# Kernel optimization log

Hardware: AMD Instinct MI355X
Metric: run time of the kernel (lower is better)

## Reference

```python
import math
import jax, jax.numpy as jnp
import numpy as np

H, KV, D = 16, 4, 128          # num_heads, num_kv_heads, head_dim
HID = 2048                      # hidden_size
ROPE_BASE = 1e6
EPS = 1e-6


def setup_inputs() -> dict:
    key = jax.random.key(0)
    ks = jax.random.split(key, 3)
    B, S = 2, 2048
    s = 0.02
    return {
        "x": jax.random.normal(ks[0], (B, S, HID), jnp.float32),
        "w_qkv": jax.random.normal(ks[1], (2 * H * D + 2 * KV * D, HID), jnp.float32) * s,
        "w_o": jax.random.normal(ks[2], (HID, H * D), jnp.float32) * s,
        "q_norm_w": jnp.ones((D,), jnp.float32),
        "q_norm_b": jnp.zeros((D,), jnp.float32),
        "k_norm_w": jnp.ones((D,), jnp.float32),
        "k_norm_b": jnp.zeros((D,), jnp.float32),
    }


def _layernorm(x, w, b):
    mu = jnp.mean(x, axis=-1, keepdims=True)
    xc = x - mu
    var = jnp.mean(xc * xc, axis=-1, keepdims=True)
    return xc * jax.lax.rsqrt(var + EPS) * w + b


def _rope(x, cos, sin):
    # x: [B, h, S, D]; cos/sin: [S, D/2]; interleaved real/imag pairs
    xr, xi = x[..., 0::2], x[..., 1::2]
    c, s = cos[None, None], sin[None, None]
    out = jnp.stack([xr * c - xi * s, xr * s + xi * c], axis=-1)
    return out.reshape(x.shape)


def reference(x, w_qkv, w_o, q_norm_w, q_norm_b, k_norm_w, k_norm_b):
    B, S, _ = x.shape
    qkv = x @ w_qkv.T                                  # [B,S,2*H*D+2*KV*D]
    qg, k, v = jnp.split(qkv, [2 * H * D, 2 * H * D + KV * D], axis=-1)
    q, gate = jnp.split(qg, 2, axis=-1)                # [B,S,H*D] each

    q = q.reshape(B, S, H, D).transpose(0, 2, 1, 3)    # [B,H,S,D]
    k = k.reshape(B, S, KV, D).transpose(0, 2, 1, 3)   # [B,KV,S,D]
    v = v.reshape(B, S, KV, D).transpose(0, 2, 1, 3)

    q = _layernorm(q, q_norm_w, q_norm_b)
    k = _layernorm(k, k_norm_w, k_norm_b)

    inv = 1.0 / (ROPE_BASE ** (jnp.arange(0, D, 2, dtype=jnp.float32) / D))
    freqs = jnp.outer(jnp.arange(S, dtype=jnp.float32), inv)  # [S, D/2]
    cos, sin = jnp.cos(freqs), jnp.sin(freqs)
    q = _rope(q, cos, sin)
    k = _rope(k, cos, sin)

    rep = H // KV
    k = jnp.repeat(k, rep, axis=1)                     # [B,H,S,D]
    v = jnp.repeat(v, rep, axis=1)

    scores = jnp.einsum('bhqd,bhkd->bhqk', q, k) / math.sqrt(D)
    causal = jnp.tril(jnp.ones((S, S), bool))
    scores = jnp.where(causal[None, None], scores, -jnp.inf)
    attn = jax.nn.softmax(scores, axis=-1)
    out = jnp.einsum('bhqk,bhkd->bhqd', attn, v)
    out = out.transpose(0, 2, 1, 3).reshape(B, S, H * D)
    out = out * jax.nn.sigmoid(gate)
    return out @ w_o.T
```

## Files before the change

### kernel.cpp

```cpp
#include <hip/hip_runtime.h>
#include <hip/hip_bf16.h>

typedef __bf16 bf16_t;
typedef __bf16 bf16x2 __attribute__((ext_vector_type(2)));
typedef __bf16 bf16x4v __attribute__((ext_vector_type(4)));
typedef __bf16 bf16x8 __attribute__((ext_vector_type(8)));
typedef float f32x4 __attribute__((ext_vector_type(4)));

#define LOG2E 1.4426950408889634f
#define QSCALE (0.08838834764831843f * 1.4426950408889634f)

__global__ __launch_bounds__(256) void cvt_f32_bf16(const float* __restrict__ in,
                                                    bf16_t* __restrict__ out, int n4) {
  int i = blockIdx.x * 256 + threadIdx.x;
  if (i < n4) {
    float4 v = ((const float4*)in)[i];
    bf16x4v o;
    o[0] = (__bf16)v.x; o[1] = (__bf16)v.y; o[2] = (__bf16)v.z; o[3] = (__bf16)v.w;
    *(bf16x4v*)(out + (size_t)i * 4) = o;
  }
}

__global__ __launch_bounds__(256) void rope_tables(float* __restrict__ cosT,
                                                   float* __restrict__ sinT) {
  int idx = blockIdx.x * 256 + threadIdx.x;
  int s = idx >> 6, i = idx & 63;
  float inv = __builtin_amdgcn_exp2f(-(float)i * (19.931568569324174f / 64.0f));
  float f = (float)s * inv;
  cosT[idx] = cosf(f);
  sinT[idx] = sinf(f);
}

template<int MI, int NI>
__global__ __launch_bounds__(512) void gemm8p(const bf16_t* __restrict__ A,
                                              const bf16_t* __restrict__ B,
                                              float* __restrict__ C,
                                              int M, int N, int K) {
  constexpr int BM = MI * 32;
  constexpr int BN = NI * 64;
  constexpr int NA = BM / 64;
  constexpr int NB = BN / 64;
  constexpr int ST = NA + NB;
  constexpr int PH = MI / 2;

  __shared__ bf16_t LA[2][BM * 64];
  __shared__ bf16_t LB[2][BN * 64];

  int nb = N / BN;
  int cpx = gridDim.x >> 3;
  int bid = blockIdx.x;
  int swz = (bid & 7) * cpx + (bid >> 3);
  int bm = swz / nb, bn = swz % nb;
  int m0 = bm * BM, n0 = bn * BN;
  int tid = threadIdx.x, lane = tid & 63, wv = tid >> 6;
  int wr = wv >> 2, wc = wv & 3, lr = lane & 15, g = lane >> 4;
  int T = K >> 6;

  auto stageI = [&](int kt, int bi, int s) {
    int k0 = kt << 6;
    if (s < NA) {
      int c = s * 512 + tid;
      int row = c >> 3, lc = (c & 7) ^ (row & 7);
      __builtin_amdgcn_global_load_lds(
          (const __attribute__((address_space(1))) void*)(A + (size_t)(m0 + row) * K + k0 + lc * 8),
          (__attribute__((address_space(3))) void*)&LA[bi][(s * 512 + wv * 64) * 8], 16, 0, 0);
    } else {
      int c = (s - NA) * 512 + tid;
      int row = c >> 3, lc = (c & 7) ^ (row & 7);
      __builtin_amdgcn_global_load_lds(
          (const __attribute__((address_space(1))) void*)(B + (size_t)(n0 + row) * K + k0 + lc * 8),
          (__attribute__((address_space(3))) void*)&LB[bi][((s - NA) * 512 + wv * 64) * 8], 16, 0, 0);
    }
  };

  f32x4 acc[MI][NI];
#pragma unroll
  for (int i = 0; i < MI; i++)
#pragma unroll
    for (int j = 0; j < NI; j++)
#pragma unroll
      for (int r = 0; r < 4; r++) acc[i][j][r] = 0.f;

#pragma unroll
  for (int s = 0; s < ST; s++) stageI(0, 0, s);

  int ofk0 = ((0 + g) ^ (lr & 7)) << 3;
  int ofk1 = ((4 + g) ^ (lr & 7)) << 3;
  int offA = (wr * (MI * 16) + lr) * 64;
  int offB = (wc * (NI * 16) + lr) * 64;

  for (int t = 0; t < T; t++) {
    int bi = t & 1, bo = bi ^ 1;
    const bf16_t* la = LA[bi];
    const bf16_t* lb = LB[bi];
    bool pre = (t + 1 < T);
    if (pre) {
#pragma unroll
      for (int s = 0; s < ST; s++) stageI(t + 1, bo, s);
      if constexpr (ST == 9) asm volatile("s_waitcnt vmcnt(9)" ::: "memory");
      else                   asm volatile("s_waitcnt vmcnt(6)" ::: "memory");
    } else {
      asm volatile("s_waitcnt vmcnt(0)" ::: "memory");
    }
    __builtin_amdgcn_s_barrier();
    asm volatile("" ::: "memory");
    bf16x8 bq[NI];
#pragma unroll
    for (int ph = 0; ph < PH; ph++) {
      const int ks = (PH == 4) ? (ph >> 1) : ph;
      const int q  = (PH == 4) ? (ph & 1) : 0;
      const bool rb = (PH == 2) || ((ph & 1) == 0);
      const int ofk = ks ? ofk1 : ofk0;
      bf16x8 af[4];
#pragma unroll
      for (int i = 0; i < 4; i++)
        af[i] = *(const bf16x8*)&la[offA + (q * 4 + i) * 1024 + ofk];
      if (rb) {
#pragma unroll
        for (int ni = 0; ni < NI; ni++)
          bq[ni] = *(const bf16x8*)&lb[offB + ni * 1024 + ofk];
      }
      if (ph != 0) {
        asm volatile("" ::: "memory");
        __builtin_amdgcn_s_barrier();
        asm volatile("" ::: "memory");
      }
      __builtin_amdgcn_s_setprio(1);
#pragma unroll
      for (int i = 0; i < 4; i++)
#pragma unroll
        for (int ni = 0; ni < NI; ni++)
          acc[q * 4 + i][ni] =
              __builtin_amdgcn_mfma_f32_16x16x32_bf16(af[i], bq[ni], acc[q * 4 + i][ni], 0, 0, 0);
      __builtin_amdgcn_s_setprio(0);
      asm volatile("s_waitcnt lgkmcnt(0)" ::: "memory");
      __builtin_amdgcn_s_barrier();
      asm volatile("" ::: "memory");
    }
  }

#pragma unroll
  for (int mi = 0; mi < MI; mi++)
#pragma unroll
    for (int ni = 0; ni < NI; ni++) {
      int m = m0 + wr * (MI * 16) + mi * 16 + g * 4;
      int n = n0 + wc * (NI * 16) + ni * 16 + lr;
#pragma unroll
      for (int r = 0; r < 4; r++) C[(size_t)(m + r) * N + n] = acc[mi][ni][r];
    }
}

__global__ __launch_bounds__(256) void ln_rope(const float* __restrict__ qkv,
                                               const float* __restrict__ qw, const float* __restrict__ qb,
                                               const float* __restrict__ kw, const float* __restrict__ kb,
                                               const float* __restrict__ cosT, const float* __restrict__ sinT,
                                               bf16_t* __restrict__ Qr, bf16_t* __restrict__ Kr) {
  int row = blockIdx.x;
  int b = row >> 11, s = row & 2047;
  int lane = threadIdx.x & 63, wv = threadIdx.x >> 6;
  float c = cosT[(s << 6) + lane], sn = sinT[(s << 6) + lane];
  const float* base = qkv + (size_t)row * 5120;
#pragma unroll
  for (int i = 0; i < 5; i++) {
    int head = wv * 5 + i;
    bool isq = head < 16;
    int off = isq ? (head << 7) : (4096 + ((head - 16) << 7));
    float2 x = *(const float2*)(base + off + (lane << 1));
    float sum = x.x + x.y;
#pragma unroll
    for (int m = 1; m < 64; m <<= 1) sum += __shfl_xor(sum, m);
    float mu = sum * 0.0078125f;
    float x0 = x.x - mu, x1 = x.y - mu;
    float vs = x0 * x0 + x1 * x1;
#pragma unroll
    for (int m = 1; m < 64; m <<= 1) vs += __shfl_xor(vs, m);
    float rs = rsqrtf(vs * 0.0078125f + 1e-6f);
    const float* w = isq ? qw : kw;
    const float* bb = isq ? qb : kb;
    float y0 = x0 * rs * w[lane << 1] + bb[lane << 1];
    float y1 = x1 * rs * w[(lane << 1) + 1] + bb[(lane << 1) + 1];
    float o0 = y0 * c - y1 * sn;
    float o1 = y0 * sn + y1 * c;
    if (isq) { o0 *= QSCALE; o1 *= QSCALE; }
    bf16x2 ov; ov[0] = (__bf16)o0; ov[1] = (__bf16)o1;
    size_t dst = isq ? ((((size_t)(b * 16 + head)) * 2048 + s) * 128 + (lane << 1))
                     : ((((size_t)(b * 4 + (head - 16))) * 2048 + s) * 128 + (lane << 1));
    *(bf16x2*)((isq ? Qr : Kr) + dst) = ov;
  }
}

__global__ __launch_bounds__(256) void vtrans(const float* __restrict__ qkv,
                                              bf16_t* __restrict__ Vt) {
  int bid = blockIdx.x;
  int sb = bid & 63, kv = (bid >> 6) & 3, b = bid >> 8;
  int s0 = sb << 5;
  __shared__ bf16_t T[128 * 33];
  int tid = threadIdx.x;
#pragma unroll
  for (int i = 0; i < 16; i++) {
    int idx = i * 256 + tid;
    int r = idx >> 7, d = idx & 127;
    float v = qkv[((size_t)(b * 2048 + s0 + r)) * 5120 + 4608 + (kv << 7) + d];
    T[d * 33 + r] = (__bf16)v;
  }
  __syncthreads();
#pragma unroll
  for (int j = 0; j < 16; j++) {
    int idx = j * 256 + tid;
    int d = idx >> 5, sc = idx & 31;
    Vt[(((size_t)(b * 4 + kv)) * 128 + d) * 2048 + s0 + sc] = T[d * 33 + sc];
  }
}

__global__ __launch_bounds__(256, 3) void attn(const bf16_t* __restrict__ Qr,
                                               const bf16_t* __restrict__ Kr,
                                               const bf16_t* __restrict__ Vt,
                                               const float* __restrict__ qkv,
                                               bf16_t* __restrict__ ag) {
  __shared__ bf16_t Ks[2][32 * 128];
  __shared__ bf16_t Vs[2][128 * 32];
  int bid = blockIdx.x;
  int hb = bid & 31;
  int h = hb & 15, b = hb >> 4;
  int pr = bid >> 5;
  int kvh = h >> 2;
  int tid = threadIdx.x, lane = tid & 63, wv = tid >> 6;
  int lr = lane & 15, g = lane >> 4;
  int r0base = ((lr >> 2) << 3) + (lr & 3);

  const bf16_t* Kg = Kr + ((size_t)(b * 4 + kvh)) * 2048 * 128;
  const bf16_t* Vg = Vt + ((size_t)(b * 4 + kvh)) * 128 * 2048;

  auto stage = [&](int buf, int kv0) {
#pragma unroll
    for (int i = 0; i < 2; i++) {
      int c = i * 256 + tid;
      int row = c >> 4, lc = (c & 15) ^ (row & 15);
      __builtin_amdgcn_global_load_lds(
          (const __attribute__((address_space(1))) void*)(Kg + (size_t)(kv0 + row) * 128 + lc * 8),
          (__attribute__((address_space(3))) void*)&Ks[buf][c * 8], 16, 0, 0);
    }
#pragma unroll
    for (int i = 0; i < 2; i++) {
      int c = i * 256 + tid;
      int d = c >> 2, cv = (c & 3) ^ ((d >> 1) & 3);
      __builtin_amdgcn_global_load_lds(
          (const __attribute__((address_space(1))) void*)(Vg + (size_t)d * 2048 + kv0 + cv * 8),
          (__attribute__((address_space(3))) void*)&Vs[buf][c * 8], 16, 0, 0);
    }
  };

  auto sm = [&](const f32x4& s0, const f32x4& s1, int qrow, int kvabs, bool dia,
                float& mrun, float& lsp, bf16x8& pb, f32x4 (&oac)[8]) {
    float tt[8];
#pragma unroll
    for (int r = 0; r < 4; r++) { tt[r] = s0[r]; tt[4 + r] = s1[r]; }
    if (dia) {
#pragma unroll
      for (int r = 0; r < 4; r++) {
        if (kvabs + r > qrow)     tt[r]     = -1e30f;
        if (kvabs + 4 + r > qrow) tt[4 + r] = -1e30f;
      }
    }
    float lm = fmaxf(fmaxf(fmaxf(tt[0], tt[1]), tt[2]),
                     fmaxf(fmaxf(tt[3], tt[4]), fmaxf(fmaxf(tt[5], tt[6]), tt[7])));
    if (__all(lm <= mrun + 8.f)) {
      float ps = 0.f;
#pragma unroll
      for (int i = 0; i < 8; i++) {
        float pv = __builtin_amdgcn_exp2f(tt[i] - mrun);
        pb[i] = (__bf16)pv; ps += pv;
      }
      lsp += ps;
    } else {
      float pm = lm;
      pm = fmaxf(pm, __shfl_xor(pm, 16));
      pm = fmaxf(pm, __shfl_xor(pm, 32));
      float mnew = fmaxf(mrun, pm);
      float corr = __builtin_amdgcn_exp2f(mrun - mnew);
      float ps = 0.f;
#pragma unroll
      for (int i = 0; i < 8; i++) {
        float pv = __builtin_amdgcn_exp2f(tt[i] - mnew);
        pb[i] = (__bf16)pv; ps += pv;
      }
      lsp = lsp * corr + ps;
      mrun = mnew;
#pragma unroll
      for (int dt = 0; dt < 8; dt++)
#pragma unroll
        for (int r = 0; r < 4; r++) oac[dt][r] *= corr;
    }
  };

  for (int phase = 0; phase < 2; phase++) {
    int qb = phase ? (31 - pr) : pr;
    int qw0 = qb << 6;
    int qw = qw0 + (wv << 4);
    int qrow = qw + lr;
    int qmax = qw + 15;
    int nt = (qb + 1) << 1;

    const bf16_t* Qg = Qr + (((size_t)(b * 16 + h)) * 2048 + qrow) * 128;
    bf16x8 qf[4];
#pragma unroll
    for (int ds = 0; ds < 4; ds++) qf[ds] = *(const bf16x8*)(Qg + ds * 32 + g * 8);

    f32x4 oa[8];
#pragma unroll
    for (int i = 0; i < 8; i++)
#pragma unroll
      for (int r = 0; r < 4; r++) oa[i][r] = 0.f;
    float mrun = -1e30f, lsp = 0.f;

    stage(0, 0);
    for (int t = 0; t < nt; t++) {
      int cur = t & 1;
      if (t + 1 < nt) {
        stage(cur ^ 1, (t + 1) << 5);
        asm volatile("s_waitcnt vmcnt(4)" ::: "memory");
      } else {
        asm volatile("s_waitcnt vmcnt(0)" ::: "memory");
      }
      __builtin_amdgcn_s_barrier();
      asm volatile("" ::: "memory");
      int kvb = t << 5;
      if (kvb <= qmax) {
        const bf16_t* kb = Ks[cur];
        const bf16_t* vb = Vs[cur];
        int ra = r0base, rb2 = r0base + 4;
        bf16x8 a0[4], a1[4];
#pragma unroll
        for (int ds = 0; ds < 4; ds++) {
          a0[ds] = *(const bf16x8*)&kb[ra * 128 + (((ds * 4 + g) ^ (ra & 15)) << 3)];
          a1[ds] = *(const bf16x8*)&kb[rb2 * 128 + (((ds * 4 + g) ^ (rb2 & 15)) << 3)];
        }
        f32x4 s0, s1;
#pragma unroll
        for (int r = 0; r < 4; r++) { s0[r] = 0.f; s1[r] = 0.f; }
        __builtin_amdgcn_s_setprio(1);
#pragma unroll
        for (int ds = 0; ds < 4; ds++) {
          s0 = __builtin_amdgcn_mfma_f32_16x16x32_bf16(a0[ds], qf[ds], s0, 0, 0, 0);
          s1 = __builtin_amdgcn_mfma_f32_16x16x32_bf16(a1[ds], qf[ds], s1, 0, 0, 0);
        }
        __builtin_amdgcn_s_setprio(0);
        int kvabs = kvb + (g << 3);
        bool dia = (kvb + 31 > qw);
        bf16x8 pb;
        sm(s0, s1, qrow, kvabs, dia, mrun, lsp, pb, oa);
        __builtin_amdgcn_s_setprio(1);
#pragma unroll
        for (int dt = 0; dt < 8; dt++) {
          int d = dt * 16 + lr;
          bf16x8 va = *(const bf16x8*)&vb[d * 32 + ((g ^ ((d >> 1) & 3)) << 3)];
          oa[dt] = __builtin_amdgcn_mfma_f32_16x16x32_bf16(va, pb, oa[dt], 0, 0, 0);
        }
        __builtin_amdgcn_s_setprio(0);
      }
      asm volatile("s_waitcnt lgkmcnt(0)" ::: "memory");
      __builtin_amdgcn_s_barrier();
      asm volatile("" ::: "memory");
    }

    float ls = lsp + __shfl_xor(lsp, 16);
    ls += __shfl_xor(ls, 32);
    float invl = __builtin_amdgcn_rcpf(ls);

    size_t ob = ((size_t)b * 2048 + qrow) * 2048 + (h << 7);
    size_t gb = ((size_t)b * 2048 + qrow) * 5120 + 2048 + (h << 7);
#pragma unroll
    for (int dt = 0; dt < 8; dt++) {
      int d = dt * 16 + (g << 2);
      float4 gt = *(const float4*)(qkv + gb + d);
      bf16x4v o;
      o[0] = (__bf16)(oa[dt][0] * invl * __builtin_amdgcn_rcpf(1.f + __builtin_amdgcn_exp2f(-gt.x * LOG2E)));
      o[1] = (__bf16)(oa[dt][1] * invl * __builtin_amdgcn_rcpf(1.f + __builtin_amdgcn_exp2f(-gt.y * LOG2E)));
      o[2] = (__bf16)(oa[dt][2] * invl * __builtin_amdgcn_rcpf(1.f + __builtin_amdgcn_exp2f(-gt.z * LOG2E)));
      o[3] = (__bf16)(oa[dt][3] * invl * __builtin_amdgcn_rcpf(1.f + __builtin_amdgcn_exp2f(-gt.w * LOG2E)));
      *(bf16x4v*)(ag + ob + d) = o;
    }
  }
}

extern "C" void kernel_launch(void* const* d_in, const int* in_sizes, int n_in,
                              void* d_out, int out_size, void* d_ws, size_t ws_size,
                              hipStream_t stream) {
  const float* x    = (const float*)d_in[0];
  const float* wqkv = (const float*)d_in[1];
  const float* wo   = (const float*)d_in[2];
  const float* qnw  = (const float*)d_in[3];
  const float* qnb  = (const float*)d_in[4];
  const float* knw  = (const float*)d_in[5];
  const float* knb  = (const float*)d_in[6];
  float* out = (float*)d_out;

  char* p = (char*)d_ws;
  bf16_t* xb  = (bf16_t*)p;
  bf16_t* ag  = xb;
  p += (size_t)16777216;
  bf16_t* wqb = (bf16_t*)p;
  bf16_t* Qr  = wqb;
  p += (size_t)20971520;
  bf16_t* wob = (bf16_t*)p; p += (size_t)8388608;
  float*  qkv = (float*)p;  p += (size_t)83886080;
  bf16_t* Kr  = (bf16_t*)p; p += (size_t)4194304;
  bf16_t* Vt  = (bf16_t*)p; p += (size_t)4194304;
  float* cosT = (float*)p;  p += (size_t)524288;
  float* sinT = (float*)p;  p += (size_t)524288;

  cvt_f32_bf16<<<8192, 256, 0, stream>>>(x, xb, 2097152);
  cvt_f32_bf16<<<10240, 256, 0, stream>>>(wqkv, wqb, 2621440);
  cvt_f32_bf16<<<4096, 256, 0, stream>>>(wo, wob, 1048576);
  rope_tables<<<512, 256, 0, stream>>>(cosT, sinT);

  gemm8p<8, 5><<<256, 512, 0, stream>>>(xb, wqb, qkv, 4096, 5120, 2048);

  ln_rope<<<4096, 256, 0, stream>>>(qkv, qnw, qnb, knw, knb, cosT, sinT, Qr, Kr);
  vtrans<<<512, 256, 0, stream>>>(qkv, Vt);

  attn<<<512, 256, 0, stream>>>(Qr, Kr, Vt, qkv, ag);

  gemm8p<4, 4><<<256, 512, 0, stream>>>(ag, wob, out, 4096, 2048, 2048);
}
```

Baseline: 255.0 us.

## Restructure GEMM into four-phase ping-pong schedule with register prefetch of fragments

Replaces the templated 8-phase GEMM with a fixed BM=128 kernel whose K-step runs in four MFMA phases. LDS fragment reads for the next phase and the next tile are issued before the current MFMAs, so shared-memory latency overlaps compute. Global loads for tile t+1 are now waited on with vmcnt(0) only at the end of the iteration. The QKV projection moves from 256-row tiles on 256 blocks to 128-row tiles on 512 blocks, which adds tile count and reuses each loaded tile less.

New measurement: 287.6 us. 1.13x slower.

```diff
diff --git a/kernel.cpp b/kernel.cpp
--- a/kernel.cpp
+++ b/kernel.cpp
@@ -31,17 +31,16 @@
   sinT[idx] = sinf(f);
 }
 
-template<int MI, int NI>
-__global__ __launch_bounds__(512) void gemm8p(const bf16_t* __restrict__ A,
+template<int NI>
+__global__ __launch_bounds__(512) void gemm4p(const bf16_t* __restrict__ A,
                                               const bf16_t* __restrict__ B,
                                               float* __restrict__ C,
                                               int M, int N, int K) {
-  constexpr int BM = MI * 32;
+  constexpr int BM = 128;
   constexpr int BN = NI * 64;
-  constexpr int NA = BM / 64;
-  constexpr int NB = BN / 64;
+  constexpr int NA = 2;
+  constexpr int NB = NI;
   constexpr int ST = NA + NB;
-  constexpr int PH = MI / 2;
 
   __shared__ bf16_t LA[2][BM * 64];
   __shared__ bf16_t LB[2][BN * 64];
@@ -73,77 +72,103 @@
     }
   };
 
-  f32x4 acc[MI][NI];
-#pragma unroll
-  for (int i = 0; i < MI; i++)
+  f32x4 acc[4][NI];
+#pragma unroll
+  for (int i = 0; i < 4; i++)
 #pragma unroll
     for (int j = 0; j < NI; j++)
 #pragma unroll
       for (int r = 0; r < 4; r++) acc[i][j][r] = 0.f;
-
-#pragma unroll
-  for (int s = 0; s < ST; s++) stageI(0, 0, s);
 
   int ofk0 = ((0 + g) ^ (lr & 7)) << 3;
   int ofk1 = ((4 + g) ^ (lr & 7)) << 3;
-  int offA = (wr * (MI * 16) + lr) * 64;
+  int offA = (wr * 64 + lr) * 64;
   int offB = (wc * (NI * 16) + lr) * 64;
+
+#pragma unroll
+  for (int s = 0; s < ST; s++) stageI(0, 0, s);
+  asm volatile("s_waitcnt vmcnt(0)" ::: "memory");
+  __builtin_amdgcn_s_barrier();
+  asm volatile("" ::: "memory");
+
+  bf16x8 afA[2], afB[2], bqA[NI], bqB[NI];
+#pragma unroll
+  for (int i = 0; i < 2; i++) afA[i] = *(const bf16x8*)&LA[0][offA + i * 1024 + ofk0];
+#pragma unroll
+  for (int ni = 0; ni < NI; ni++) bqA[ni] = *(const bf16x8*)&LB[0][offB + ni * 1024 + ofk0];
 
   for (int t = 0; t < T; t++) {
     int bi = t & 1, bo = bi ^ 1;
     const bf16_t* la = LA[bi];
     const bf16_t* lb = LB[bi];
+    const bf16_t* lan = LA[bo];
+    const bf16_t* lbn = LB[bo];
     bool pre = (t + 1 < T);
+
     if (pre) {
 #pragma unroll
       for (int s = 0; s < ST; s++) stageI(t + 1, bo, s);
-      if constexpr (ST == 9) asm volatile("s_waitcnt vmcnt(9)" ::: "memory");
-      else                   asm volatile("s_waitcnt vmcnt(6)" ::: "memory");
-    } else {
-      asm volatile("s_waitcnt vmcnt(0)" ::: "memory");
-    }
+    }
+#pragma unroll
+    for (int i = 0; i < 2; i++) afB[i] = *(const bf16x8*)&la[offA + (2 + i) * 1024 + ofk0];
+    __builtin_amdgcn_s_setprio(1);
+#pragma unroll
+    for (int i = 0; i < 2; i++)
+#pragma unroll
+      for (int ni = 0; ni < NI; ni++)
+        acc[i][ni] = __builtin_amdgcn_mfma_f32_16x16x32_bf16(afA[i], bqA[ni], acc[i][ni], 0, 0, 0);
+    __builtin_amdgcn_s_setprio(0);
+    __builtin_amdgcn_s_barrier();
+
+#pragma unroll
+    for (int i = 0; i < 2; i++) afA[i] = *(const bf16x8*)&la[offA + i * 1024 + ofk1];
+#pragma unroll
+    for (int ni = 0; ni < NI; ni++) bqB[ni] = *(const bf16x8*)&lb[offB + ni * 1024 + ofk1];
+    __builtin_amdgcn_s_setprio(1);
+#pragma unroll
+    for (int i = 0; i < 2; i++)
+#pragma unroll
+      for (int ni = 0; ni < NI; ni++)
+        acc[2 + i][ni] = __builtin_amdgcn_mfma_f32_16x16x32_bf16(afB[i], bqA[ni], acc[2 + i][ni], 0, 0, 0);
+    __builtin_amdgcn_s_setprio(0);
+    __builtin_amdgcn_s_barrier();
+
+#pragma unroll
+    for (int i = 0; i < 2; i++) afB[i] = *(const bf16x8*)&la[offA + (2 + i) * 1024 + ofk1];
+    __builtin_amdgcn_s_setprio(1);
+#pragma unroll
+    for (int i = 0; i < 2; i++)
+#pragma unroll
+      for (int ni = 0; ni < NI; ni++)
+        acc[i][ni] = __builtin_amdgcn_mfma_f32_16x16x32_bf16(afA[i], bqB[ni], acc[i][ni], 0, 0, 0);
+    __builtin_amdgcn_s_setprio(0);
+    __builtin_amdgcn_s_barrier();
+
+    if (pre) asm volatile("s_waitcnt vmcnt(0)" ::: "memory");
     __builtin_amdgcn_s_barrier();
     asm volatile("" ::: "memory");
-    bf16x8 bq[NI];
-#pragma unroll
-    for (int ph = 0; ph < PH; ph++) {
-      const int ks = (PH == 4) ? (ph >> 1) : ph;
-      const int q  = (PH == 4) ? (ph & 1) : 0;
-      const bool rb = (PH == 2) || ((ph & 1) == 0);
-      const int ofk = ks ? ofk1 : ofk0;
-      bf16x8 af[4];
-#pragma unroll
-      for (int i = 0; i < 4; i++)
-        af[i] = *(const bf16x8*)&la[offA + (q * 4 + i) * 1024 + ofk];
-      if (rb) {
-#pragma unroll
-        for (int ni = 0; ni < NI; ni++)
-          bq[ni] = *(const bf16x8*)&lb[offB + ni * 1024 + ofk];
-      }
-      if (ph != 0) {
-        asm volatile("" ::: "memory");
-        __builtin_amdgcn_s_barrier();
-        asm volatile("" ::: "memory");
-      }
-      __builtin_amdgcn_s_setprio(1);
-#pragma unroll
-      for (int i = 0; i < 4; i++)
-#pragma unroll
-        for (int ni = 0; ni < NI; ni++)
-          acc[q * 4 + i][ni] =
-              __builtin_amdgcn_mfma_f32_16x16x32_bf16(af[i], bq[ni], acc[q * 4 + i][ni], 0, 0, 0);
-      __builtin_amdgcn_s_setprio(0);
-      asm volatile("s_waitcnt lgkmcnt(0)" ::: "memory");
-      __builtin_amdgcn_s_barrier();
-      asm volatile("" ::: "memory");
-    }
-  }
-
-#pragma unroll
-  for (int mi = 0; mi < MI; mi++)
+    if (pre) {
+#pragma unroll
+      for (int i = 0; i < 2; i++) afA[i] = *(const bf16x8*)&lan[offA + i * 1024 + ofk0];
+#pragma unroll
+      for (int ni = 0; ni < NI; ni++) bqA[ni] = *(const bf16x8*)&lbn[offB + ni * 1024 + ofk0];
+    }
+    __builtin_amdgcn_s_setprio(1);
+#pragma unroll
+    for (int i = 0; i < 2; i++)
+#pragma unroll
+      for (int ni = 0; ni < NI; ni++)
+        acc[2 + i][ni] = __builtin_amdgcn_mfma_f32_16x16x32_bf16(afB[i], bqB[ni], acc[2 + i][ni], 0, 0, 0);
+    __builtin_amdgcn_s_setprio(0);
+    __builtin_amdgcn_s_barrier();
+    asm volatile("" ::: "memory");
+  }
+
+#pragma unroll
+  for (int mi = 0; mi < 4; mi++)
 #pragma unroll
     for (int ni = 0; ni < NI; ni++) {
-      int m = m0 + wr * (MI * 16) + mi * 16 + g * 4;
+      int m = m0 + wr * 64 + mi * 16 + g * 4;
       int n = n0 + wc * (NI * 16) + ni * 16 + lr;
 #pragma unroll
       for (int r = 0; r < 4; r++) C[(size_t)(m + r) * N + n] = acc[mi][ni][r];
@@ -414,12 +439,12 @@
   cvt_f32_bf16<<<4096, 256, 0, stream>>>(wo, wob, 1048576);
   rope_tables<<<512, 256, 0, stream>>>(cosT, sinT);
 
-  gemm8p<8, 5><<<256, 512, 0, stream>>>(xb, wqb, qkv, 4096, 5120, 2048);
+  gemm4p<5><<<512, 512, 0, stream>>>(xb, wqb, qkv, 4096, 5120, 2048);
 
   ln_rope<<<4096, 256, 0, stream>>>(qkv, qnw, qnb, knw, knb, cosT, sinT, Qr, Kr);
   vtrans<<<512, 256, 0, stream>>>(qkv, Vt);
 
   attn<<<512, 256, 0, stream>>>(Qr, Kr, Vt, qkv, ag);
 
-  gemm8p<4, 4><<<256, 512, 0, stream>>>(ag, wob, out, 4096, 2048, 2048);
-}
+  gemm4p<4><<<256, 512, 0, stream>>>(ag, wob, out, 4096, 2048, 2048);
+}
```

## Store QKV projection in bf16 and simplify GEMM inner loop barriers

Applied to the files above, without the earlier changes.

The QKV GEMM now writes its output as bf16 instead of fp32, halving the 80MB intermediate write and the reads by ln_rope, vtrans and the attention gate. Consumers are retyped to read bf16 and upcast. Separately, the GEMM k-loop drops the phased per-step barriers and setprio. It loads both k-halves of B fragments once and issues all MFMAs with a single barrier per tile. This adds precision loss on Q/K/V/gate before layernorm and changes register pressure and scheduling in the GEMM.

Measured after the change: 236.5 us. 1.08x faster.

```diff
diff --git a/kernel.cpp b/kernel.cpp
--- a/kernel.cpp
+++ b/kernel.cpp
@@ -31,17 +31,16 @@
   sinT[idx] = sinf(f);
 }
 
-template<int MI, int NI>
+template<int MI, int NI, typename OT>
 __global__ __launch_bounds__(512) void gemm8p(const bf16_t* __restrict__ A,
                                               const bf16_t* __restrict__ B,
-                                              float* __restrict__ C,
+                                              OT* __restrict__ C,
                                               int M, int N, int K) {
   constexpr int BM = MI * 32;
   constexpr int BN = NI * 64;
   constexpr int NA = BM / 64;
   constexpr int NB = BN / 64;
   constexpr int ST = NA + NB;
-  constexpr int PH = MI / 2;
 
   __shared__ bf16_t LA[2][BM * 64];
   __shared__ bf16_t LB[2][BN * 64];
@@ -104,39 +103,38 @@
     }
     __builtin_amdgcn_s_barrier();
     asm volatile("" ::: "memory");
-    bf16x8 bq[NI];
-#pragma unroll
-    for (int ph = 0; ph < PH; ph++) {
-      const int ks = (PH == 4) ? (ph >> 1) : ph;
-      const int q  = (PH == 4) ? (ph & 1) : 0;
-      const bool rb = (PH == 2) || ((ph & 1) == 0);
-      const int ofk = ks ? ofk1 : ofk0;
-      bf16x8 af[4];
+
+    bf16x8 bq0[NI], bq1[NI];
+#pragma unroll
+    for (int ni = 0; ni < NI; ni++) bq0[ni] = *(const bf16x8*)&lb[offB + ni * 1024 + ofk0];
+#pragma unroll
+    for (int ni = 0; ni < NI; ni++) bq1[ni] = *(const bf16x8*)&lb[offB + ni * 1024 + ofk1];
+#pragma unroll
+    for (int q = 0; q < MI / 4; q++) {
+      bf16x8 af0[4], af1[4];
 #pragma unroll
       for (int i = 0; i < 4; i++)
-        af[i] = *(const bf16x8*)&la[offA + (q * 4 + i) * 1024 + ofk];
-      if (rb) {
-#pragma unroll
-        for (int ni = 0; ni < NI; ni++)
-          bq[ni] = *(const bf16x8*)&lb[offB + ni * 1024 + ofk];
-      }
-      if (ph != 0) {
-        asm volatile("" ::: "memory");
-        __builtin_amdgcn_s_barrier();
-        asm volatile("" ::: "memory");
-      }
-      __builtin_amdgcn_s_setprio(1);
+        af0[i] = *(const bf16x8*)&la[offA + (q * 4 + i) * 1024 + ofk0];
 #pragma unroll
       for (int i = 0; i < 4; i++)
 #pragma unroll
         for (int ni = 0; ni < NI; ni++)
           acc[q * 4 + i][ni] =
-              __builtin_amdgcn_mfma_f32_16x16x32_bf16(af[i], bq[ni], acc[q * 4 + i][ni], 0, 0, 0);
-      __builtin_amdgcn_s_setprio(0);
-      asm volatile("s_waitcnt lgkmcnt(0)" ::: "memory");
-      __builtin_amdgcn_s_barrier();
-      asm volatile("" ::: "memory");
-    }
+              __builtin_amdgcn_mfma_f32_16x16x32_bf16(af0[i], bq0[ni], acc[q * 4 + i][ni], 0, 0, 0);
+#pragma unroll
+      for (int i = 0; i < 4; i++)
+        af1[i] = *(const bf16x8*)&la[offA + (q * 4 + i) * 1024 + ofk1];
+#pragma unroll
+      for (int i = 0; i < 4; i++)
+#pragma unroll
+        for (int ni = 0; ni < NI; ni++)
+          acc[q * 4 + i][ni] =
+              __builtin_amdgcn_mfma_f32_16x16x32_bf16(af1[i], bq1[ni], acc[q * 4 + i][ni], 0, 0, 0);
+    }
+
+    asm volatile("s_waitcnt lgkmcnt(0)" ::: "memory");
+    __builtin_amdgcn_s_barrier();
+    asm volatile("" ::: "memory");
   }
 
 #pragma unroll
@@ -146,11 +144,11 @@
       int m = m0 + wr * (MI * 16) + mi * 16 + g * 4;
       int n = n0 + wc * (NI * 16) + ni * 16 + lr;
 #pragma unroll
-      for (int r = 0; r < 4; r++) C[(size_t)(m + r) * N + n] = acc[mi][ni][r];
-    }
-}
-
-__global__ __launch_bounds__(256) void ln_rope(const float* __restrict__ qkv,
+      for (int r = 0; r < 4; r++) C[(size_t)(m + r) * N + n] = (OT)acc[mi][ni][r];
+    }
+}
+
+__global__ __launch_bounds__(256) void ln_rope(const bf16_t* __restrict__ qkv,
                                                const float* __restrict__ qw, const float* __restrict__ qb,
                                                const float* __restrict__ kw, const float* __restrict__ kb,
                                                const float* __restrict__ cosT, const float* __restrict__ sinT,
@@ -159,18 +157,19 @@
   int b = row >> 11, s = row & 2047;
   int lane = threadIdx.x & 63, wv = threadIdx.x >> 6;
   float c = cosT[(s << 6) + lane], sn = sinT[(s << 6) + lane];
-  const float* base = qkv + (size_t)row * 5120;
+  const bf16_t* base = qkv + (size_t)row * 5120;
 #pragma unroll
   for (int i = 0; i < 5; i++) {
     int head = wv * 5 + i;
     bool isq = head < 16;
     int off = isq ? (head << 7) : (4096 + ((head - 16) << 7));
-    float2 x = *(const float2*)(base + off + (lane << 1));
-    float sum = x.x + x.y;
+    bf16x2 xv = *(const bf16x2*)(base + off + (lane << 1));
+    float x0f = (float)xv[0], x1f = (float)xv[1];
+    float sum = x0f + x1f;
 #pragma unroll
     for (int m = 1; m < 64; m <<= 1) sum += __shfl_xor(sum, m);
     float mu = sum * 0.0078125f;
-    float x0 = x.x - mu, x1 = x.y - mu;
+    float x0 = x0f - mu, x1 = x1f - mu;
     float vs = x0 * x0 + x1 * x1;
 #pragma unroll
     for (int m = 1; m < 64; m <<= 1) vs += __shfl_xor(vs, m);
@@ -189,7 +188,7 @@
   }
 }
 
-__global__ __launch_bounds__(256) void vtrans(const float* __restrict__ qkv,
+__global__ __launch_bounds__(256) void vtrans(const bf16_t* __restrict__ qkv,
                                               bf16_t* __restrict__ Vt) {
   int bid = blockIdx.x;
   int sb = bid & 63, kv = (bid >> 6) & 3, b = bid >> 8;
@@ -200,8 +199,7 @@
   for (int i = 0; i < 16; i++) {
     int idx = i * 256 + tid;
     int r = idx >> 7, d = idx & 127;
-    float v = qkv[((size_t)(b * 2048 + s0 + r)) * 5120 + 4608 + (kv << 7) + d];
-    T[d * 33 + r] = (__bf16)v;
+    T[d * 33 + r] = qkv[((size_t)(b * 2048 + s0 + r)) * 5120 + 4608 + (kv << 7) + d];
   }
   __syncthreads();
 #pragma unroll
@@ -215,7 +213,7 @@
 __global__ __launch_bounds__(256, 3) void attn(const bf16_t* __restrict__ Qr,
                                                const bf16_t* __restrict__ Kr,
                                                const bf16_t* __restrict__ Vt,
-                                               const float* __restrict__ qkv,
+                                               const bf16_t* __restrict__ qkv,
                                                bf16_t* __restrict__ ag) {
   __shared__ bf16_t Ks[2][32 * 128];
   __shared__ bf16_t Vs[2][128 * 32];
@@ -372,12 +370,12 @@
 #pragma unroll
     for (int dt = 0; dt < 8; dt++) {
       int d = dt * 16 + (g << 2);
-      float4 gt = *(const float4*)(qkv + gb + d);
+      bf16x4v gt = *(const bf16x4v*)(qkv + gb + d);
       bf16x4v o;
-      o[0] = (__bf16)(oa[dt][0] * invl * __builtin_amdgcn_rcpf(1.f + __builtin_amdgcn_exp2f(-gt.x * LOG2E)));
-      o[1] = (__bf16)(oa[dt][1] * invl * __builtin_amdgcn_rcpf(1.f + __builtin_amdgcn_exp2f(-gt.y * LOG2E)));
-      o[2] = (__bf16)(oa[dt][2] * invl * __builtin_amdgcn_rcpf(1.f + __builtin_amdgcn_exp2f(-gt.z * LOG2E)));
-      o[3] = (__bf16)(oa[dt][3] * invl * __builtin_amdgcn_rcpf(1.f + __builtin_amdgcn_exp2f(-gt.w * LOG2E)));
+      o[0] = (__bf16)(oa[dt][0] * invl * __builtin_amdgcn_rcpf(1.f + __builtin_amdgcn_exp2f(-(float)gt[0] * LOG2E)));
+      o[1] = (__bf16)(oa[dt][1] * invl * __builtin_amdgcn_rcpf(1.f + __builtin_amdgcn_exp2f(-(float)gt[1] * LOG2E)));
+      o[2] = (__bf16)(oa[dt][2] * invl * __builtin_amdgcn_rcpf(1.f + __builtin_amdgcn_exp2f(-(float)gt[2] * LOG2E)));
+      o[3] = (__bf16)(oa[dt][3] * invl * __builtin_amdgcn_rcpf(1.f + __builtin_amdgcn_exp2f(-(float)gt[3] * LOG2E)));
       *(bf16x4v*)(ag + ob + d) = o;
     }
   }
@@ -403,7 +401,7 @@
   bf16_t* Qr  = wqb;
   p += (size_t)20971520;
   bf16_t* wob = (bf16_t*)p; p += (size_t)8388608;
-  float*  qkv = (float*)p;  p += (size_t)83886080;
+  bf16_t* qkv = (bf16_t*)p; p += (size_t)41943040;
   bf16_t* Kr  = (bf16_t*)p; p += (size_t)4194304;
   bf16_t* Vt  = (bf16_t*)p; p += (size_t)4194304;
   float* cosT = (float*)p;  p += (size_t)524288;
@@ -414,12 +412,12 @@
   cvt_f32_bf16<<<4096, 256, 0, stream>>>(wo, wob, 1048576);
   rope_tables<<<512, 256, 0, stream>>>(cosT, sinT);
 
-  gemm8p<8, 5><<<256, 512, 0, stream>>>(xb, wqb, qkv, 4096, 5120, 2048);
+  gemm8p<8, 5, bf16_t><<<256, 512, 0, stream>>>(xb, wqb, qkv, 4096, 5120, 2048);
 
   ln_rope<<<4096, 256, 0, stream>>>(qkv, qnw, qnb, knw, knb, cosT, sinT, Qr, Kr);
   vtrans<<<512, 256, 0, stream>>>(qkv, Vt);
 
   attn<<<512, 256, 0, stream>>>(Qr, Kr, Vt, qkv, ag);
 
-  gemm8p<4, 4><<<256, 512, 0, stream>>>(ag, wob, out, 4096, 2048, 2048);
-}
+  gemm8p<4, 4, float><<<256, 512, 0, stream>>>(ag, wob, out, 4096, 2048, 2048);
+}
```
